# Optimization experiments

Hardware: AMD Instinct MI355X
Metric: run time of the kernel (lower is better)

The kernel has to match this reference:

```python
import jax, jax.numpy as jnp
import numpy as np

FEATURE_DIM = 512
NUM_HEADS = 8
HEAD_DIM = FEATURE_DIM // NUM_HEADS


def setup_inputs() -> dict:
    key = jax.random.key(0)
    ks = jax.random.split(key, 16)
    B, N, F = 16, 768, FEATURE_DIM
    Nb = N // 3
    s = 1.0 / np.sqrt(F)
    inp = {
        "x_1": jax.random.normal(ks[0], (B, N, F), jnp.float32),
        "x_2": jax.random.normal(ks[1], (B, N, F), jnp.float32),
        "z_b": jax.random.normal(ks[2], (Nb, F), jnp.float32),
        # weights stored [in, out] (torch Linear applies x @ W.T)
        "Wqkv_i": jax.random.normal(ks[3], (F, 3 * F), jnp.float32) * s,
        "Wqkv_j": jax.random.normal(ks[4], (F, 3 * F), jnp.float32) * s,
        "Wqkv_b": jax.random.normal(ks[5], (F, 3 * F), jnp.float32) * s,
        "W_f": jax.random.normal(ks[6], (2 * F, F), jnp.float32) * s,
        "b_f": jnp.zeros((F,), jnp.float32),
        "W_m": jax.random.normal(ks[7], (F, F), jnp.float32) * s,
        "b_m": jnp.zeros((F,), jnp.float32),
        "W_QKV": jax.random.normal(ks[8], (F, 3 * F), jnp.float32) * s,
        "W_proj": jax.random.normal(ks[9], (F, F), jnp.float32) * s,
        "b_proj": jnp.zeros((F,), jnp.float32),
    }
    return inp


def reference(x_1, x_2, z_b, Wqkv_i, Wqkv_j, Wqkv_b, W_f, b_f, W_m, b_m, W_QKV, W_proj, b_proj):
    z_i, z_j = x_1, x_2
    B, N, F = z_i.shape
    Nb = z_b.shape[0]
    scale = F ** -0.5           # full-dim attention scale
    Scale = HEAD_DIM ** -0.5    # multi-head attention scale

    zb = jnp.broadcast_to((z_b * 0.2)[None], (B, Nb, F))

    def split_qkv(x, W):
        qkv = (x @ W).reshape(x.shape[0], x.shape[1], 3, F)
        return qkv[:, :, 0], qkv[:, :, 1], qkv[:, :, 2]

    _, k_i, v_i = split_qkv(z_i, Wqkv_i)
    q_j, _, _ = split_qkv(z_j, Wqkv_j)
    q_b, k_b, v_b = split_qkv(zb, Wqkv_b)

    # bottleneck cross attentions (single-head, full feature dim)
    a_ib = jax.nn.softmax(jnp.einsum('bmf,bnf->bmn', q_b, k_i) * scale, axis=-1)  # [B,Nb,N]
    a_bj = jax.nn.softmax(jnp.einsum('bnf,bmf->bnm', q_j, k_b) * scale, axis=-1)  # [B,N,Nb]

    a_ib = jnp.einsum('bmn,bnf->bmf', a_ib, v_i)  # [B,Nb,F]
    attn_up = jax.nn.softmax(jnp.einsum('bnf,bmf->bnm', z_i, a_ib) * scale, axis=-1)  # [B,N,Nb]
    a_ib = jnp.einsum('bnm,bmf->bnf', attn_up, a_ib)  # [B,N,F]
    a_bj = jnp.einsum('bnm,bmf->bnf', a_bj, v_b)      # [B,N,F]
    a_ij = (a_ib + a_bj) * 0.5

    # gated fusion
    f_ij = jax.nn.sigmoid(jnp.concatenate([a_ij, z_j], axis=-1) @ W_f + b_f)
    h_ij = jax.nn.relu(z_i + (a_ij @ W_m + b_m) * f_ij)

    # standard multi-head self-attention
    QKV = (h_ij @ W_QKV).reshape(B, N, 3, NUM_HEADS, HEAD_DIM)
    Q, K, V = [jnp.transpose(QKV[:, :, t], (0, 2, 1, 3)) for t in range(3)]  # [B,H,N,hd]
    Attn = jax.nn.softmax(jnp.einsum('bhnd,bhmd->bhnm', Q, K) * Scale, axis=-1)
    H = jnp.einsum('bhnm,bhmd->bhnd', Attn, V)
    H = jnp.transpose(H, (0, 2, 1, 3)).reshape(B, N, F)
    return H @ W_proj + b_proj
```

## Files before the change

### kernel.cpp

```cpp
#include <hip/hip_runtime.h>
#include <hip/hip_bf16.h>

typedef __attribute__((ext_vector_type(8))) short short8;
typedef __attribute__((ext_vector_type(4))) float f32x4;
typedef __hip_bfloat16 bf16;
typedef unsigned short ushort;

__device__ __forceinline__ ushort f2b(float v) {
    bf16 h = __float2bfloat16(v);
    return *reinterpret_cast<ushort*>(&h);
}
__device__ __forceinline__ float b2f(ushort u) {
    return __uint_as_float((unsigned)u << 16);
}

#define GLD16(lds, gp) __builtin_amdgcn_global_load_lds( \
    (const __attribute__((address_space(1))) void*)(gp), \
    (__attribute__((address_space(3))) void*)(lds), 16, 0, 0)

__device__ __forceinline__ void xcd_swizzle(int& bx, int& by) {
    if ((gridDim.y & 7) == 0) {
        const int id = bx + gridDim.x * by;
        const int xcd = id & 7, slot = id >> 3;
        by = xcd * (gridDim.y >> 3) + slot / gridDim.x;
        bx = slot - (slot / gridDim.x) * gridDim.x;
    }
}

template<typename OutT, int EPI, int TM>
__global__ __launch_bounds__(256) void gemm_bf16(
    const bf16* __restrict__ A, const bf16* __restrict__ B, OutT* __restrict__ C,
    int K, int lda, int ldb, int ldc, long sA, long sB, long sC,
    float alpha, const float* __restrict__ bias,
    int lda2, long sA2, int eld, long sE,
    bf16* __restrict__ px, bf16* __restrict__ py, int nry)
{
    constexpr int RT = TM / 32;
    constexpr int PLA = TM * 32;
    constexpr int PLB = 128 * 32;
    constexpr int NP = (TM == 64) ? 4 : 2;
    __shared__ __align__(16) bf16 As[NP * PLA];
    __shared__ __align__(16) bf16 Bs[NP * PLB];

    const int t = threadIdx.x;
    const int w = t >> 6, lane = t & 63;
    const int wr = w >> 1, wc = w & 1;
    const int lr = lane & 15, kc4 = lane >> 4;
    const int qr = lane >> 2;
    const int kcr = ((lane & 3) - ((lane >> 3) & 3)) & 3;
    int bx = blockIdx.x, by = blockIdx.y;
    xcd_swizzle(bx, by);
    int zidx, row0;
    if (nry > 0) { zidx = by / nry; row0 = (by % nry) * TM; }
    else         { zidx = blockIdx.z; row0 = by * TM; }
    const int col0 = bx * 128;

    const bf16* Ab = A + (size_t)zidx * sA + (size_t)row0 * lda;
    const bf16* Bb = B + (size_t)zidx * sB + (size_t)col0 * ldb;

    const bf16* ga0; const bf16* ga1 = nullptr;
    if constexpr (TM == 64) {
        ga0 = Ab + (size_t)(w * 16 + qr) * lda + kcr * 8;
    } else {
        ga0 = Ab + (size_t)(w * 32 + qr) * lda + kcr * 8;
        ga1 = Ab + (size_t)(w * 32 + 16 + qr) * lda + kcr * 8;
    }
    const bf16* gb0 = Bb + (size_t)(w * 32 + qr) * ldb + kcr * 8;
    const bf16* gb1 = Bb + (size_t)(w * 32 + 16 + qr) * ldb + kcr * 8;
    bf16* lA0; bf16* lA1 = nullptr;
    if constexpr (TM == 64) { lA0 = &As[w * 512]; }
    else                    { lA0 = &As[w * 1024]; lA1 = &As[w * 1024 + 512]; }
    bf16* lB0 = &Bs[w * 1024];
    bf16* lB1 = &Bs[w * 1024 + 512];

    f32x4 acc[RT][4] = {};

    const int cSw = ((kc4 + ((lr >> 1) & 3)) & 3) * 8;
    const bf16* ApBase = &As[(wr * (TM / 2) + lr) * 32 + cSw];
    const bf16* BpBase = &Bs[(wc * 64 + lr) * 32 + cSw];

    auto stageP = [&](int plane, int ko) {
        GLD16(lA0 + plane * PLA, ga0 + ko);
        if constexpr (TM == 128) GLD16(lA1 + plane * PLA, ga1 + ko);
        GLD16(lB0 + plane * PLB, gb0 + ko);
        GLD16(lB1 + plane * PLB, gb1 + ko);
    };
    auto compP = [&](int plane) {
        const bf16* Ap = ApBase + plane * PLA;
        const bf16* Bp = BpBase + plane * PLB;
        short8 af[RT], bfr[4];
#pragma unroll
        for (int i = 0; i < RT; ++i) af[i]  = *(const short8*)(Ap + i * 512);
#pragma unroll
        for (int j = 0; j < 4; ++j) bfr[j] = *(const short8*)(Bp + j * 512);
#pragma unroll
        for (int i = 0; i < RT; ++i)
#pragma unroll
            for (int j = 0; j < 4; ++j)
                acc[i][j] = __builtin_amdgcn_mfma_f32_16x16x32_bf16(af[i], bfr[j], acc[i][j], 0, 0, 0);
    };

    if constexpr (TM == 64) {
        stageP(0, 0); stageP(1, 32);
        int buf = 0;
        for (int k0 = 0; k0 < K; k0 += 64) {
            __syncthreads();
            if (k0 + 64 < K) {
                stageP((buf ^ 1) * 2,     k0 + 64);
                stageP((buf ^ 1) * 2 + 1, k0 + 96);
            }
            compP(buf * 2); compP(buf * 2 + 1);
            buf ^= 1;
        }
    } else {
        stageP(0, 0);
        int buf = 0;
        for (int k0 = 0; k0 < K; k0 += 32) {
            __syncthreads();
            if (k0 + 32 < K) stageP(buf ^ 1, k0 + 32);
            compP(buf);
            buf ^= 1;
        }
    }

    if constexpr (EPI == 4) {
        const int sec = bx >> 2;
        const int h0 = (bx & 3) * 2;
        const int b  = by / 6;
        const int n0 = (by % 6) * TM;
        bf16* dq = (bf16*)C;
#pragma unroll
        for (int j = 0; j < 4; ++j) {
            const int col = wc * 64 + j * 16 + lr;
            const int h = h0 + (col >> 6), hd = col & 63;
            const size_t bh = (size_t)b * 8 + h;
#pragma unroll
            for (int i = 0; i < RT; ++i) {
                const int n = n0 + wr * (TM / 2) + i * 16 + kc4 * 4;
                if (sec == 2) {
                    __align__(8) ushort o[4];
#pragma unroll
                    for (int r = 0; r < 4; ++r) o[r] = f2b(acc[i][j][r]);
                    *(int2*)&py[(bh * 64 + hd) * 768 + n] = *(const int2*)o;
                } else {
                    bf16* d = (sec == 0) ? dq : px;
#pragma unroll
                    for (int r = 0; r < 4; ++r)
                        d[(bh * 768 + n + r) * 64 + hd] = __float2bfloat16(acc[i][j][r]);
                }
            }
        }
        return;
    } else if constexpr (EPI == 5) {
        const int b  = by / 6;
        const int n0 = (by % 6) * TM;
#pragma unroll
        for (int j = 0; j < 4; ++j) {
            const int col = col0 + wc * 64 + j * 16 + lr;
#pragma unroll
            for (int i = 0; i < RT; ++i) {
                const int n = n0 + wr * (TM / 2) + i * 16 + kc4 * 4;
                if (col < 512) {
#pragma unroll
                    for (int r = 0; r < 4; ++r)
                        ((bf16*)C)[((size_t)b * 768 + n + r) * 512 + col] = __float2bfloat16(acc[i][j][r]);
                } else {
                    __align__(8) ushort o[4];
#pragma unroll
                    for (int r = 0; r < 4; ++r) o[r] = f2b(acc[i][j][r]);
                    *(int2*)&py[((size_t)b * 512 + (col - 512)) * 768 + n] = *(const int2*)o;
                }
            }
        }
        return;
    }

    OutT* Cb = C + (size_t)zidx * sC;
#pragma unroll
    for (int j = 0; j < 4; ++j) {
        const int col = col0 + wc * 64 + j * 16 + lr;
        const float bv = bias ? bias[col] : 0.f;
#pragma unroll
        for (int i = 0; i < RT; ++i) {
            const int rb = row0 + wr * (TM / 2) + i * 16 + kc4 * 4;
            if constexpr (EPI == 6) {
                __align__(8) ushort o[4];
#pragma unroll
                for (int r = 0; r < 4; ++r) {
                    o[r] = f2b(alpha * acc[i][j][r]);
                    Cb[(size_t)(rb + r) * ldc + col] = __float2bfloat16(alpha * acc[i][j][r]);
                }
                *(int2*)&py[(size_t)zidx * sE + (size_t)col * eld + rb] = *(const int2*)o;
            } else if constexpr (EPI == 8) {
                __align__(8) ushort o[4];
#pragma unroll
                for (int r = 0; r < 4; ++r) {
                    o[r] = f2b(acc[i][j][r]);
                    Cb[(size_t)(rb + r) * ldc + col] = __float2bfloat16(acc[i][j][r]);
                }
                if (col >= 1024) {
                    const size_t tb = (size_t)(col - 1024) * 512 + 256 + rb;
#pragma unroll
                    for (int b2 = 0; b2 < 16; ++b2)
                        *(int2*)&py[(size_t)b2 * sE + tb] = *(const int2*)o;
                }
            } else {
#pragma unroll
                for (int r = 0; r < 4; ++r) {
                    const int row = rb + r;
                    float v = alpha * acc[i][j][r] + bv;
                    if constexpr (sizeof(OutT) == 2)
                        Cb[(size_t)row * ldc + col] = __float2bfloat16(v);
                    else
                        Cb[(size_t)row * ldc + col] = v;
                }
            }
        }
    }
}

__global__ __launch_bounds__(256) void gemm_sm(
    const bf16* __restrict__ A0, const bf16* __restrict__ B0,
    const bf16* __restrict__ A1, const bf16* __restrict__ B1,
    bf16* __restrict__ Y, float alpha)
{
    constexpr int PLA = 64 * 32;
    constexpr int PLB = 256 * 32;
    __shared__ __align__(16) bf16 As[2 * PLA];
    __shared__ __align__(16) bf16 Bs[2 * PLB];
    __shared__ float sc[2][2][2][32];

    const int t = threadIdx.x;
    const int w = t >> 6, lane = t & 63;
    const int wr = w >> 1, wc = w & 1;
    const int lr = lane & 15, kc4 = lane >> 4;
    const int qr = lane >> 2;
    const int kcr = ((lane & 3) - ((lane >> 3) & 3)) & 3;
    int bx = blockIdx.x, by = blockIdx.y;
    xcd_swizzle(bx, by);
    const int b = by / 12, row0 = (by % 12) * 64;
    const int half = blockIdx.z;

    const bf16* Ab; int lda; const bf16* Bb;
    if (half == 0) {
        Ab = A0 + (size_t)b * (768L * 512) + (size_t)row0 * 512;  lda = 512;
        Bb = B0 + (size_t)b * (256L * 512);
    } else {
        Ab = A1 + (size_t)b * (768L * 1024) + (size_t)row0 * 1024; lda = 1024;
        Bb = B1;
    }

    const bf16* ga0 = Ab + (size_t)(w * 16 + qr) * lda + kcr * 8;
    const bf16* gb0 = Bb + (size_t)(w * 32 + qr) * 512 + kcr * 8;
    const bf16* gb1 = Bb + (size_t)(w * 32 + 16 + qr) * 512 + kcr * 8;
    const bf16* gb2 = Bb + (size_t)(128 + w * 32 + qr) * 512 + kcr * 8;
    const bf16* gb3 = Bb + (size_t)(128 + w * 32 + 16 + qr) * 512 + kcr * 8;
    bf16* lA0 = &As[w * 512];
    bf16* lB0 = &Bs[w * 1024];        bf16* lB1 = &Bs[w * 1024 + 512];
    bf16* lB2 = &Bs[4096 + w * 1024]; bf16* lB3 = &Bs[4096 + w * 1024 + 512];

    f32x4 acc[2][8] = {};

    const int cSw = ((kc4 + ((lr >> 1) & 3)) & 3) * 8;
    const bf16* ApBase = &As[(wr * 32 + lr) * 32 + cSw];
    const bf16* BpBase = &Bs[(wc * 128 + lr) * 32 + cSw];

    auto stageP = [&](int pl, int ko) {
        GLD16(lA0 + pl * PLA, ga0 + ko);
        GLD16(lB0 + pl * PLB, gb0 + ko); GLD16(lB1 + pl * PLB, gb1 + ko);
        GLD16(lB2 + pl * PLB, gb2 + ko); GLD16(lB3 + pl * PLB, gb3 + ko);
    };
    auto compP = [&](int pl) {
        const bf16* Ap = ApBase + pl * PLA;
        const bf16* Bp = BpBase + pl * PLB;
        short8 af[2], bfr[8];
#pragma unroll
        for (int i = 0; i < 2; ++i) af[i] = *(const short8*)(Ap + i * 512);
#pragma unroll
        for (int j = 0; j < 8; ++j) bfr[j] = *(const short8*)(Bp + j * 512);
#pragma unroll
        for (int i = 0; i < 2; ++i)
#pragma unroll
            for (int j = 0; j < 8; ++j)
                acc[i][j] = __builtin_amdgcn_mfma_f32_16x16x32_bf16(af[i], bfr[j], acc[i][j], 0, 0, 0);
    };

    stageP(0, 0);
    int buf = 0;
    for (int k0 = 0; k0 < 512; k0 += 32) {
        __syncthreads();
        if (k0 + 32 < 512) stageP(buf ^ 1, k0 + 32);
        compP(buf);
        buf ^= 1;
    }

    float mloc[2][4], sloc[2][4], scl[2][4];
#pragma unroll
    for (int i = 0; i < 2; ++i)
#pragma unroll
        for (int e = 0; e < 4; ++e) {
            float m = alpha * acc[i][0][e];
#pragma unroll
            for (int j = 1; j < 8; ++j) m = fmaxf(m, alpha * acc[i][j][e]);
#pragma unroll
            for (int o = 1; o < 16; o <<= 1) m = fmaxf(m, __shfl_xor(m, o));
            mloc[i][e] = m;
            float s = 0.f;
#pragma unroll
            for (int j = 0; j < 8; ++j) {
                const float p = __expf(alpha * acc[i][j][e] - m);
                acc[i][j][e] = p;
                s += p;
            }
#pragma unroll
            for (int o = 1; o < 16; o <<= 1) s += __shfl_xor(s, o);
            sloc[i][e] = s;
            if (lr == 0) {
                sc[wr][wc][0][i * 16 + kc4 * 4 + e] = m;
                sc[wr][wc][1][i * 16 + kc4 * 4 + e] = s;
            }
        }
    __syncthreads();
#pragma unroll
    for (int i = 0; i < 2; ++i)
#pragma unroll
        for (int e = 0; e < 4; ++e) {
            const float m2 = sc[wr][wc ^ 1][0][i * 16 + kc4 * 4 + e];
            const float s2 = sc[wr][wc ^ 1][1][i * 16 + kc4 * 4 + e];
            const float M = fmaxf(mloc[i][e], m2);
            const float S = sloc[i][e] * __expf(mloc[i][e] - M) + s2 * __expf(m2 - M);
            scl[i][e] = __expf(mloc[i][e] - M) / S;
        }
    bf16* dst = Y + ((size_t)b * 768 + row0) * 512 + half * 256 + wc * 128;
#pragma unroll
    for (int i = 0; i < 2; ++i)
#pragma unroll
        for (int j = 0; j < 8; ++j)
#pragma unroll
            for (int e = 0; e < 4; ++e)
                dst[(size_t)(wr * 32 + i * 16 + kc4 * 4 + e) * 512 + j * 16 + lr] =
                    __float2bfloat16(acc[i][j][e] * scl[i][e]);
}

__global__ __launch_bounds__(256) void gemm_gate(
    const bf16* __restrict__ A, const bf16* __restrict__ Bf,
    const bf16* __restrict__ Bm, bf16* __restrict__ Cout,
    const float* __restrict__ bias_f, const float* __restrict__ bias_m,
    const bf16* __restrict__ x1b)
{
    constexpr int AHW = 64 * 32;
    constexpr int BHW = 128 * 32;
    __shared__ __align__(16) bf16 As[2 * AHW];
    __shared__ __align__(16) bf16 FsS[2 * BHW];
    __shared__ __align__(16) bf16 MsS[2 * BHW];

    const int t = threadIdx.x;
    const int w = t >> 6, lane = t & 63;
    const int lr = lane & 15, kc4 = lane >> 4;
    const int qr = lane >> 2;
    const int kcr = ((lane & 3) - ((lane >> 3) & 3)) & 3;
    int bx = blockIdx.x, by = blockIdx.y;
    xcd_swizzle(bx, by);
    const int row0 = by * 64, col0 = bx * 128;

    const bf16* ga0 = A  + (size_t)(row0 + w * 16 + qr) * 1024 + kcr * 8;
    const bf16* gf0 = Bf + (size_t)(col0 + w * 32 + qr) * 1024 + kcr * 8;
    const bf16* gf1 = Bf + (size_t)(col0 + w * 32 + 16 + qr) * 1024 + kcr * 8;
    const bf16* gm0 = Bm + (size_t)(col0 + w * 32 + qr) * 512 + kcr * 8;
    const bf16* gm1 = Bm + (size_t)(col0 + w * 32 + 16 + qr) * 512 + kcr * 8;
    bf16* lA0 = &As[w * 512];
    bf16* lF0 = &FsS[w * 1024]; bf16* lF1 = &FsS[w * 1024 + 512];
    bf16* lM0 = &MsS[w * 1024]; bf16* lM1 = &MsS[w * 1024 + 512];

    f32x4 acc1[4][2] = {};
    f32x4 acc2[4][2] = {};

    const int cSw = ((kc4 + ((lr >> 1) & 3)) & 3) * 8;
    const bf16* ApBase = &As[lr * 32 + cSw];
    const bf16* FpBase = &FsS[(w * 32 + lr) * 32 + cSw];
    const bf16* MpBase = &MsS[(w * 32 + lr) * 32 + cSw];

    GLD16(lA0, ga0);
    GLD16(lF0, gf0); GLD16(lF1, gf1);
    GLD16(lM0, gm0); GLD16(lM1, gm1);

    auto step = [&](int kk, int rd, int st) {
        __syncthreads();
        const int kn = kk + 32;
        if (kn < 1024) {
            GLD16(lA0 + st * AHW, ga0 + kn);
            GLD16(lF0 + st * BHW, gf0 + kn);
            GLD16(lF1 + st * BHW, gf1 + kn);
            if (kn < 512) {
                GLD16(lM0 + st * BHW, gm0 + kn);
                GLD16(lM1 + st * BHW, gm1 + kn);
            }
        }
        const bf16* Ap = ApBase + rd * AHW;
        const bf16* Fp = FpBase + rd * BHW;
        short8 af[4], ff[2];
#pragma unroll
        for (int i = 0; i < 4; ++i) af[i] = *(const short8*)(Ap + i * 512);
#pragma unroll
        for (int j = 0; j < 2; ++j) ff[j] = *(const short8*)(Fp + j * 512);
#pragma unroll
        for (int i = 0; i < 4; ++i)
#pragma unroll
            for (int j = 0; j < 2; ++j)
                acc1[i][j] = __builtin_amdgcn_mfma_f32_16x16x32_bf16(af[i], ff[j], acc1[i][j], 0, 0, 0);
        if (kk < 512) {
            const bf16* Mp = MpBase + rd * BHW;
            short8 mf[2];
#pragma unroll
            for (int j = 0; j < 2; ++j) mf[j] = *(const short8*)(Mp + j * 512);
#pragma unroll
            for (int i = 0; i < 4; ++i)
#pragma unroll
                for (int j = 0; j < 2; ++j)
                    acc2[i][j] = __builtin_amdgcn_mfma_f32_16x16x32_bf16(af[i], mf[j], acc2[i][j], 0, 0, 0);
        }
    };

    for (int k0 = 0; k0 < 1024; k0 += 64) {
        step(k0, 0, 1);
        step(k0 + 32, 1, 0);
    }

    const ushort* xr = (const ushort*)x1b;
#pragma unroll
    for (int j = 0; j < 2; ++j) {
        const int col = col0 + w * 32 + j * 16 + lr;
        const float bvf = bias_f[col], bvm = bias_m[col];
#pragma unroll
        for (int i = 0; i < 4; ++i) {
            const int rb = row0 + i * 16 + kc4 * 4;
#pragma unroll
            for (int r = 0; r < 4; ++r) {
                const int row = rb + r;
                const float sig = 1.f / (1.f + __expf(-(acc1[i][j][r] + bvf)));
                const float rr = b2f(xr[(size_t)row * 512 + col]) + (acc2[i][j][r] + bvm) * sig;
                Cout[(size_t)row * 512 + col] = __float2bfloat16(rr > 0.f ? rr : 0.f);
            }
        }
    }
}

template<typename TI, int NSRC>
__global__ __launch_bounds__(256) void k_transpose(
    const TI* __restrict__ s0, const TI* __restrict__ s1,
    const TI* __restrict__ s2, const TI* __restrict__ s3,
    bf16* __restrict__ dst, int src_ld, int dst_ld, long sSrc, long sDst,
    int rep, long repStride)
{
    __shared__ float tile[64][65];
    const int t = threadIdx.x;
    const int c0 = blockIdx.x * 64, r0 = blockIdx.y * 64;
    const int z = blockIdx.z;
    const TI* src = s0;
    if (NSRC > 1) src = (z == 0) ? s0 : (z == 1) ? s1 : (z == 2) ? s2 : s3;
    {
        const int r = t >> 2, cq = (t & 3) * 16;
        const TI* sp = src + (size_t)z * sSrc + (size_t)(r0 + r) * src_ld + c0 + cq;
        if constexpr (sizeof(TI) == 4) {
#pragma unroll
            for (int u = 0; u < 16; u += 4) {
                float4 v = *(const float4*)((const float*)sp + u);
                tile[r][cq + u]     = v.x; tile[r][cq + u + 1] = v.y;
                tile[r][cq + u + 2] = v.z; tile[r][cq + u + 3] = v.w;
            }
        } else {
            const ushort* up = (const ushort*)sp;
            union { short8 v; ushort u[8]; } p0, p1;
            p0.v = *(const short8*)up; p1.v = *(const short8*)(up + 8);
#pragma unroll
            for (int u = 0; u < 8; ++u) {
                tile[r][cq + u]     = b2f(p0.u[u]);
                tile[r][cq + 8 + u] = b2f(p1.u[u]);
            }
        }
    }
    __syncthreads();
    const int c = t >> 2, rq = (t & 3) * 16;
    __align__(16) ushort ob[16];
#pragma unroll
    for (int u = 0; u < 16; ++u) ob[u] = f2b(tile[rq + u][c]);
    for (int rp = 0; rp < rep; ++rp) {
        bf16* dp = dst + (size_t)rp * repStride + (size_t)z * sDst + (size_t)(c0 + c) * dst_ld + r0 + rq;
        *(int4*)dp       = *(const int4*)&ob[0];
        *(int4*)(dp + 8) = *(const int4*)&ob[8];
    }
}

__global__ __launch_bounds__(256) void k_cast3(const float* __restrict__ x1,
    const float* __restrict__ x2, const float* __restrict__ zb,
    const float* __restrict__ wj,
    bf16* __restrict__ d1, bf16* __restrict__ d2, bf16* __restrict__ d3,
    bf16* __restrict__ d4)
{
    const int z = blockIdx.z;
    const float* src; bf16* dst; int ld; float scale; int n;
    if (z == 0)      { src = x1; dst = d1; ld = 512;  scale = 1.f;  n = 6291456; }
    else if (z == 1) { src = x2; dst = d2; ld = 1024; scale = 1.f;  n = 6291456; }
    else if (z == 2) { src = zb; dst = d3; ld = 512;  scale = 0.2f; n = 131072;  }
    else             { src = wj; dst = d4; ld = 512;  scale = 1.f;  n = 262144;  }
    int i = (blockIdx.x * 256 + threadIdx.x) * 8;
    if (i >= n) return;
    int si = i;
    if (z == 3) si = (i >> 9) * 1536 + (i & 511);
    float4 a = *(const float4*)(src + si), b = *(const float4*)(src + si + 4);
    __align__(16) ushort o[8];
    o[0] = f2b(a.x * scale); o[1] = f2b(a.y * scale); o[2] = f2b(a.z * scale); o[3] = f2b(a.w * scale);
    o[4] = f2b(b.x * scale); o[5] = f2b(b.y * scale); o[6] = f2b(b.z * scale); o[7] = f2b(b.w * scale);
    int row = i >> 9, col = i & 511;
    *(int4*)(dst + (size_t)row * ld + col) = *(const int4*)o;
}

template<int COLS, int MODE>
__global__ __launch_bounds__(256) void softmax_wave(const float* __restrict__ X,
                                                    bf16* __restrict__ Y)
{
    const int wv = threadIdx.x >> 6, lane = threadIdx.x & 63;
    const long row = (long)blockIdx.x * 4 + wv;
    const float* src = X + row * COLS;
    constexpr int V = COLS / 64;
    float v[V];
#pragma unroll
    for (int i = 0; i < V; ++i) v[i] = src[lane + i * 64];
    float m = v[0];
#pragma unroll
    for (int i = 1; i < V; ++i) m = fmaxf(m, v[i]);
#pragma unroll
    for (int o = 32; o; o >>= 1) m = fmaxf(m, __shfl_xor(m, o));
    float s = 0.f;
#pragma unroll
    for (int i = 0; i < V; ++i) { v[i] = __expf(v[i] - m); s += v[i]; }
#pragma unroll
    for (int o = 32; o; o >>= 1) s += __shfl_xor(s, o);
    const float inv = 1.f / s;
    bf16* dst = Y + row * COLS;
#pragma unroll
    for (int i = 0; i < V; ++i) dst[lane + i * 64] = __float2bfloat16(v[i] * inv);
}

__global__ __launch_bounds__(256) void mhsa_flash_mfma(
    const bf16* __restrict__ Qb, const bf16* __restrict__ Kb,
    const bf16* __restrict__ VT, bf16* __restrict__ Hout)
{
    constexpr int LD = 72;
    __shared__ __align__(16) ushort Qs[64 * LD];
    __shared__ __align__(16) ushort Ks[64 * LD];
    __shared__ __align__(16) ushort Vt[64 * LD];
    __shared__ __align__(16) ushort Ps[64 * LD];

    const int t = threadIdx.x;
    const int w = t >> 6, lane = t & 63;
    const int l16 = lane & 15, q4 = lane >> 4;
    const int h = blockIdx.x, b = blockIdx.y, qt = blockIdx.z;
    const size_t bh = (size_t)b * 8 + h;
    const ushort* qbase = (const ushort*)Qb + bh * 768 * 64;
    const ushort* kbase = (const ushort*)Kb + bh * 768 * 64;
    const ushort* vbase = (const ushort*)VT + bh * 64 * 768;

    const int r = t >> 2, c0 = (t & 3) * 16;

    {
        const ushort* src = qbase + (size_t)(qt * 64 + r) * 64 + c0;
        *(int4*)&Qs[r * LD + c0]     = *(const int4*)src;
        *(int4*)&Qs[r * LD + c0 + 8] = *(const int4*)(src + 8);
    }

    int4 ka0, ka1, va0, va1;
    {
        const ushort* ks = kbase + (size_t)r * 64 + c0;
        ka0 = *(const int4*)ks; ka1 = *(const int4*)(ks + 8);
        const ushort* vs = vbase + (size_t)r * 768 + c0;
        va0 = *(const int4*)vs; va1 = *(const int4*)(vs + 8);
    }
    __syncthreads();

    short8 qf0 = *(const short8*)&Qs[(w * 16 + l16) * LD + q4 * 8];
    short8 qf1 = *(const short8*)&Qs[(w * 16 + l16) * LD + 32 + q4 * 8];

    float lsum[4] = {0.f, 0.f, 0.f, 0.f};
    f32x4 acc[4] = {};

    for (int kt = 0; kt < 12; ++kt) {
        if (kt) __syncthreads();
        *(int4*)&Ks[r * LD + c0]     = ka0;
        *(int4*)&Ks[r * LD + c0 + 8] = ka1;
        *(int4*)&Vt[r * LD + c0]     = va0;
        *(int4*)&Vt[r * LD + c0 + 8] = va1;
        __syncthreads();

        if (kt < 11) {
            const ushort* ks = kbase + (size_t)((kt + 1) * 64 + r) * 64 + c0;
            ka0 = *(const int4*)ks; ka1 = *(const int4*)(ks + 8);
            const ushort* vs = vbase + (size_t)r * 768 + (kt + 1) * 64 + c0;
            va0 = *(const int4*)vs; va1 = *(const int4*)(vs + 8);
        }

        f32x4 s[4] = {};
#pragma unroll
        for (int nt = 0; nt < 4; ++nt) {
            short8 kf0 = *(const short8*)&Ks[(nt * 16 + l16) * LD + q4 * 8];
            short8 kf1 = *(const short8*)&Ks[(nt * 16 + l16) * LD + 32 + q4 * 8];
            s[nt] = __builtin_amdgcn_mfma_f32_16x16x32_bf16(qf0, kf0, s[nt], 0, 0, 0);
            s[nt] = __builtin_amdgcn_mfma_f32_16x16x32_bf16(qf1, kf1, s[nt], 0, 0, 0);
        }

#pragma unroll
        for (int nt = 0; nt < 4; ++nt) {
#pragma unroll
            for (int e = 0; e < 4; ++e) {
                const float p = __expf(s[nt][e] * 0.125f);
                lsum[e] += p;
                Ps[(w * 16 + q4 * 4 + e) * LD + nt * 16 + l16] = f2b(p);
            }
        }

        short8 pf0 = *(const short8*)&Ps[(w * 16 + l16) * LD + q4 * 8];
        short8 pf1 = *(const short8*)&Ps[(w * 16 + l16) * LD + 32 + q4 * 8];
#pragma unroll
        for (int jt = 0; jt < 4; ++jt) {
            short8 vf0 = *(const short8*)&Vt[(jt * 16 + l16) * LD + q4 * 8];
            short8 vf1 = *(const short8*)&Vt[(jt * 16 + l16) * LD + 32 + q4 * 8];
            acc[jt] = __builtin_amdgcn_mfma_f32_16x16x32_bf16(pf0, vf0, acc[jt], 0, 0, 0);
            acc[jt] = __builtin_amdgcn_mfma_f32_16x16x32_bf16(pf1, vf1, acc[jt], 0, 0, 0);
        }
    }

    const int orow = qt * 64 + w * 16 + q4 * 4;
#pragma unroll
    for (int e = 0; e < 4; ++e) {
        float l = lsum[e];
        l += __shfl_xor(l, 1);
        l += __shfl_xor(l, 2);
        l += __shfl_xor(l, 4);
        l += __shfl_xor(l, 8);
        const float inv = 1.f / l;
        const size_t rbase = ((size_t)b * 768 + orow + e) * 512 + h * 64;
#pragma unroll
        for (int jt = 0; jt < 4; ++jt)
            Hout[rbase + jt * 16 + l16] = __float2bfloat16(acc[jt][e] * inv);
    }
}

extern "C" void kernel_launch(void* const* d_in, const int* in_sizes, int n_in,
                              void* d_out, int out_size, void* d_ws, size_t ws_size,
                              hipStream_t stream)
{
    (void)in_sizes; (void)n_in; (void)out_size; (void)ws_size;
    const float* x1     = (const float*)d_in[0];
    const float* x2     = (const float*)d_in[1];
    const float* z_b    = (const float*)d_in[2];
    const float* Wqkv_i = (const float*)d_in[3];
    const float* Wqkv_j = (const float*)d_in[4];
    const float* Wqkv_b = (const float*)d_in[5];
    const float* W_f    = (const float*)d_in[6];
    const float* b_f    = (const float*)d_in[7];
    const float* W_m    = (const float*)d_in[8];
    const float* b_m    = (const float*)d_in[9];
    const float* W_QKV  = (const float*)d_in[10];
    const float* W_proj = (const float*)d_in[11];
    const float* b_proj = (const float*)d_in[12];
    float* out = (float*)d_out;

    const float scale = 0.044194173824159216f;

    char* base = (char*)d_ws;
    size_t off = 0;
    auto alloc = [&](size_t bytes) { char* r = base + off; off += (bytes + 255) & ~(size_t)255; return r; };

    char* Rq  = alloc((size_t)3 * 25165824);
    char* R1  = Rq;
    char* R2  = Rq + 25165824;
    char* R3  = Rq + 2 * 25165824;
    char* R4  = alloc(25165824);
    bf16* Wt4     = (bf16*)alloc((size_t)3 * 1536 * 512 * 2);
    bf16* Wt_f    = (bf16*)alloc(512 * 1024 * 2);
    bf16* Wt_mp   = (bf16*)alloc((size_t)2 * 512 * 512 * 2);
    bf16* Wj_bf   = (bf16*)alloc(512 * 512 * 2);
    bf16* Gbuf    = (bf16*)alloc(256 * 512 * 2);
    bf16* c_zb    = (bf16*)alloc(256 * 512 * 2);
    bf16* qkvb    = (bf16*)alloc(256 * 1536 * 2);
    bf16* aib0    = (bf16*)alloc((size_t)16 * 256 * 512 * 2);
    bf16* Bcat    = (bf16*)alloc((size_t)16 * 512 * 512 * 2);
    float* S      = (float*)alloc((size_t)16 * 256 * 768 * 4);
    bf16* Sb1     = (bf16*)alloc((size_t)16 * 256 * 768 * 2);
    bf16* Sb_cat  = (bf16*)alloc((size_t)16 * 768 * 512 * 2);
    bf16* c_cat   = (bf16*)alloc((size_t)12288 * 1024 * 2);
    bf16* hbuf    = (bf16*)alloc((size_t)12288 * 512 * 2);

    bf16* Wt_i = Wt4, *Wt_b = Wt4 + 1536 * 512,
        *Wt_qkv = Wt4 + (size_t)2 * 1536 * 512;
    bf16* Wt_m = Wt_mp, *Wt_proj = Wt_mp + 512 * 512;

    bf16*  Kc   = (bf16*)R1;
    bf16*  Qb   = (bf16*)R1;
    bf16*  Kb   = (bf16*)(R1 + 12582912);
    bf16*  v_iT = (bf16*)R2;
    bf16*  VTb  = (bf16*)R2;
    bf16*  c_x1 = (bf16*)R3;
    bf16*  Hout = (bf16*)R4;

    auto G64 = [&](const bf16* A, const bf16* B, void* C, bool outBf,
                   int M, int N, int K, int lda, int ldb, int ldc,
                   long sA, long sB, long sC, int batch, float alpha,
                   const float* bias) {
        int nry = M / 64;
        dim3 grid(N / 128, (batch > 1) ? batch * nry : nry, 1);
        if (batch == 1) nry = 0;
        if (outBf) gemm_bf16<bf16, 0, 64><<<grid, 256, 0, stream>>>(A, B, (bf16*)C, K, lda, ldb, ldc, sA, sB, sC, alpha, bias, 0, 0, 0, 0, nullptr, nullptr, nry);
        else       gemm_bf16<float, 0, 64><<<grid, 256, 0, stream>>>(A, B, (float*)C, K, lda, ldb, ldc, sA, sB, sC, alpha, bias, 0, 0, 0, 0, nullptr, nullptr, nry);
    };

    k_cast3<<<dim3(3072, 1, 4), 256, 0, stream>>>(x1, x2, z_b, Wqkv_j,
                                                  c_x1, c_cat + 512, c_zb, Wj_bf);
    k_transpose<float, 3><<<dim3(24, 8, 3), 256, 0, stream>>>(
        Wqkv_i, Wqkv_b, W_QKV, nullptr, Wt4, 1536, 512, 0, 1536L * 512, 1, 0);
    k_transpose<float, 1><<<dim3(8, 16, 1), 256, 0, stream>>>(
        W_f, nullptr, nullptr, nullptr, Wt_f, 512, 1024, 0, 0, 1, 0);
    k_transpose<float, 2><<<dim3(8, 8, 2), 256, 0, stream>>>(
        W_m, W_proj, nullptr, nullptr, Wt_mp, 512, 512, 0, 512L * 512, 1, 0);

    gemm_bf16<bf16, 8, 64><<<dim3(12, 4, 1), 256, 0, stream>>>(
        c_zb, Wt_b, qkvb, 512, 512, 512, 1536, 0, 0, 0,
        1.f, nullptr, 0, 0, 0, 512L * 512, nullptr, Bcat, 0);
    G64(qkvb + 512, Wj_bf, Gbuf, true, 256, 512, 512, 1536, 512, 512, 0, 0, 0, 1, 1.f, nullptr);
    gemm_bf16<bf16, 5, 128><<<dim3(8, 96, 1), 256, 0, stream>>>(
        c_x1, Wt_i + 512 * 512, Kc, 512, 512, 512, 512, 0, 0, 0,
        1.f, nullptr, 0, 0, 0, 0, nullptr, v_iT, 0);
    G64(qkvb, Kc, S, false, 256, 768, 512, 1536, 512, 768, 0, 768L * 512, 256L * 768, 16, scale, nullptr);
    softmax_wave<768, 0><<<1024, 256, 0, stream>>>(S, Sb1);
    gemm_bf16<bf16, 6, 64><<<dim3(4, 64, 1), 256, 0, stream>>>(
        Sb1, v_iT, aib0, 768, 768, 768, 512, 256L * 768, 512L * 768, 256L * 512,
        1.f, nullptr, 0, 0, 512, 512L * 512, nullptr, Bcat, 4);
    gemm_sm<<<dim3(1, 192, 2), 256, 0, stream>>>(c_x1, aib0, c_cat + 512, Gbuf,
                                                 Sb_cat, scale);
    G64(Sb_cat, Bcat, c_cat, true, 768, 512, 512, 512, 512, 1024,
        768L * 512, 512L * 512, 768L * 1024, 16, 0.5f, nullptr);
    gemm_gate<<<dim3(4, 192), 256, 0, stream>>>(c_cat, Wt_f, Wt_m, hbuf, b_f, b_m, c_x1);
    gemm_bf16<bf16, 4, 128><<<dim3(12, 96, 1), 256, 0, stream>>>(
        hbuf, Wt_qkv, Qb, 512, 512, 512, 0, 0, 0, 0,
        1.f, nullptr, 0, 0, 0, 0, Kb, VTb, 0);
    mhsa_flash_mfma<<<dim3(8, 16, 12), 256, 0, stream>>>(Qb, Kb, VTb, Hout);
    G64(Hout, Wt_proj, out, false, 12288, 512, 512, 512, 512, 512, 0, 0, 0, 1, 1.f, b_proj);
}
```

Before: 383.4 us.

## Load GEMM B operand directly from global memory, merge weight transposes

Adds a BD template mode to the bf16 GEMM in which the B (weight) fragments are read straight from global/L2 into registers instead of staged through LDS. This cuts LDS footprint and global-to-LDS traffic for small, heavily reused weight matrices, and the gate kernel's W_m path gets the same treatment. The three weight-transpose launches are merged into one kernel with early-exit blocks. The cost is higher global-load latency inside the MFMA loop with no prefetch, which may stall compute.

```diff
diff --git a/kernel.cpp b/kernel.cpp
--- a/kernel.cpp
+++ b/kernel.cpp
@@ -27,7 +27,7 @@
     }
 }
 
-template<typename OutT, int EPI, int TM>
+template<typename OutT, int EPI, int TM, bool BD = false>
 __global__ __launch_bounds__(256) void gemm_bf16(
     const bf16* __restrict__ A, const bf16* __restrict__ B, OutT* __restrict__ C,
     int K, int lda, int ldb, int ldc, long sA, long sB, long sC,
@@ -39,8 +39,9 @@
     constexpr int PLA = TM * 32;
     constexpr int PLB = 128 * 32;
     constexpr int NP = (TM == 64) ? 4 : 2;
+    constexpr int NBS = BD ? 16 : NP * PLB;
     __shared__ __align__(16) bf16 As[NP * PLA];
-    __shared__ __align__(16) bf16 Bs[NP * PLB];
+    __shared__ __align__(16) bf16 Bs[NBS];
 
     const int t = threadIdx.x;
     const int w = t >> 6, lane = t & 63;
@@ -70,29 +71,39 @@
     bf16* lA0; bf16* lA1 = nullptr;
     if constexpr (TM == 64) { lA0 = &As[w * 512]; }
     else                    { lA0 = &As[w * 1024]; lA1 = &As[w * 1024 + 512]; }
-    bf16* lB0 = &Bs[w * 1024];
-    bf16* lB1 = &Bs[w * 1024 + 512];
+    bf16* lB0 = nullptr; bf16* lB1 = nullptr;
+    if constexpr (!BD) { lB0 = &Bs[w * 1024]; lB1 = &Bs[w * 1024 + 512]; }
 
     f32x4 acc[RT][4] = {};
 
     const int cSw = ((kc4 + ((lr >> 1) & 3)) & 3) * 8;
     const bf16* ApBase = &As[(wr * (TM / 2) + lr) * 32 + cSw];
-    const bf16* BpBase = &Bs[(wc * 64 + lr) * 32 + cSw];
+    const bf16* BpBase = nullptr;
+    if constexpr (!BD) BpBase = &Bs[(wc * 64 + lr) * 32 + cSw];
+    const bf16* gBf = Bb + (size_t)(wc * 64 + lr) * ldb + kc4 * 8;
 
     auto stageP = [&](int plane, int ko) {
         GLD16(lA0 + plane * PLA, ga0 + ko);
         if constexpr (TM == 128) GLD16(lA1 + plane * PLA, ga1 + ko);
-        GLD16(lB0 + plane * PLB, gb0 + ko);
-        GLD16(lB1 + plane * PLB, gb1 + ko);
+        if constexpr (!BD) {
+            GLD16(lB0 + plane * PLB, gb0 + ko);
+            GLD16(lB1 + plane * PLB, gb1 + ko);
+        }
     };
-    auto compP = [&](int plane) {
+    auto compP = [&](int plane, int kk) {
         const bf16* Ap = ApBase + plane * PLA;
-        const bf16* Bp = BpBase + plane * PLB;
         short8 af[RT], bfr[4];
 #pragma unroll
         for (int i = 0; i < RT; ++i) af[i]  = *(const short8*)(Ap + i * 512);
-#pragma unroll
-        for (int j = 0; j < 4; ++j) bfr[j] = *(const short8*)(Bp + j * 512);
+        if constexpr (BD) {
+#pragma unroll
+            for (int j = 0; j < 4; ++j)
+                bfr[j] = *(const short8*)(gBf + (size_t)j * 16 * ldb + kk);
+        } else {
+            const bf16* Bp = BpBase + plane * PLB;
+#pragma unroll
+            for (int j = 0; j < 4; ++j) bfr[j] = *(const short8*)(Bp + j * 512);
+        }
 #pragma unroll
         for (int i = 0; i < RT; ++i)
 #pragma unroll
@@ -109,7 +120,7 @@
                 stageP((buf ^ 1) * 2,     k0 + 64);
                 stageP((buf ^ 1) * 2 + 1, k0 + 96);
             }
-            compP(buf * 2); compP(buf * 2 + 1);
+            compP(buf * 2, k0); compP(buf * 2 + 1, k0 + 32);
             buf ^= 1;
         }
     } else {
@@ -118,7 +129,7 @@
         for (int k0 = 0; k0 < K; k0 += 32) {
             __syncthreads();
             if (k0 + 32 < K) stageP(buf ^ 1, k0 + 32);
-            compP(buf);
+            compP(buf, k0);
             buf ^= 1;
         }
     }
@@ -352,7 +363,6 @@
     constexpr int BHW = 128 * 32;
     __shared__ __align__(16) bf16 As[2 * AHW];
     __shared__ __align__(16) bf16 FsS[2 * BHW];
-    __shared__ __align__(16) bf16 MsS[2 * BHW];
 
     const int t = threadIdx.x;
     const int w = t >> 6, lane = t & 63;
@@ -366,11 +376,8 @@
     const bf16* ga0 = A  + (size_t)(row0 + w * 16 + qr) * 1024 + kcr * 8;
     const bf16* gf0 = Bf + (size_t)(col0 + w * 32 + qr) * 1024 + kcr * 8;
     const bf16* gf1 = Bf + (size_t)(col0 + w * 32 + 16 + qr) * 1024 + kcr * 8;
-    const bf16* gm0 = Bm + (size_t)(col0 + w * 32 + qr) * 512 + kcr * 8;
-    const bf16* gm1 = Bm + (size_t)(col0 + w * 32 + 16 + qr) * 512 + kcr * 8;
     bf16* lA0 = &As[w * 512];
     bf16* lF0 = &FsS[w * 1024]; bf16* lF1 = &FsS[w * 1024 + 512];
-    bf16* lM0 = &MsS[w * 1024]; bf16* lM1 = &MsS[w * 1024 + 512];
 
     f32x4 acc1[4][2] = {};
     f32x4 acc2[4][2] = {};
@@ -378,11 +385,10 @@
     const int cSw = ((kc4 + ((lr >> 1) & 3)) & 3) * 8;
     const bf16* ApBase = &As[lr * 32 + cSw];
     const bf16* FpBase = &FsS[(w * 32 + lr) * 32 + cSw];
-    const bf16* MpBase = &MsS[(w * 32 + lr) * 32 + cSw];
+    const bf16* gMf = Bm + (size_t)(col0 + w * 32 + lr) * 512 + kc4 * 8;
 
     GLD16(lA0, ga0);
     GLD16(lF0, gf0); GLD16(lF1, gf1);
-    GLD16(lM0, gm0); GLD16(lM1, gm1);
 
     auto step = [&](int kk, int rd, int st) {
         __syncthreads();
@@ -391,10 +397,6 @@
             GLD16(lA0 + st * AHW, ga0 + kn);
             GLD16(lF0 + st * BHW, gf0 + kn);
             GLD16(lF1 + st * BHW, gf1 + kn);
-            if (kn < 512) {
-                GLD16(lM0 + st * BHW, gm0 + kn);
-                GLD16(lM1 + st * BHW, gm1 + kn);
-            }
         }
         const bf16* Ap = ApBase + rd * AHW;
         const bf16* Fp = FpBase + rd * BHW;
@@ -409,10 +411,10 @@
             for (int j = 0; j < 2; ++j)
                 acc1[i][j] = __builtin_amdgcn_mfma_f32_16x16x32_bf16(af[i], ff[j], acc1[i][j], 0, 0, 0);
         if (kk < 512) {
-            const bf16* Mp = MpBase + rd * BHW;
             short8 mf[2];
 #pragma unroll
-            for (int j = 0; j < 2; ++j) mf[j] = *(const short8*)(Mp + j * 512);
+            for (int j = 0; j < 2; ++j)
+                mf[j] = *(const short8*)(gMf + (size_t)j * 16 * 512 + kk);
 #pragma unroll
             for (int i = 0; i < 4; ++i)
 #pragma unroll
@@ -445,38 +447,34 @@
     }
 }
 
-template<typename TI, int NSRC>
-__global__ __launch_bounds__(256) void k_transpose(
-    const TI* __restrict__ s0, const TI* __restrict__ s1,
-    const TI* __restrict__ s2, const TI* __restrict__ s3,
-    bf16* __restrict__ dst, int src_ld, int dst_ld, long sSrc, long sDst,
-    int rep, long repStride)
+__global__ __launch_bounds__(256) void k_transpose_all(
+    const float* __restrict__ Wi, const float* __restrict__ Wb,
+    const float* __restrict__ Wq, const float* __restrict__ Wf,
+    const float* __restrict__ Wm, const float* __restrict__ Wp,
+    bf16* __restrict__ dWt4, bf16* __restrict__ dWf, bf16* __restrict__ dWmp)
 {
+    const int z = blockIdx.z;
+    const float* src; bf16* dst; int sld, dld, xmax, ymax;
+    if (z < 3)      { src = (z == 0) ? Wi : (z == 1) ? Wb : Wq;
+                      dst = dWt4 + (size_t)z * 1536 * 512;
+                      sld = 1536; dld = 512; xmax = 24; ymax = 8; }
+    else if (z == 3){ src = Wf; dst = dWf; sld = 512; dld = 1024; xmax = 8; ymax = 16; }
+    else            { src = (z == 4) ? Wm : Wp;
+                      dst = dWmp + (size_t)(z - 4) * 512 * 512;
+                      sld = 512; dld = 512; xmax = 8; ymax = 8; }
+    if (blockIdx.x >= (unsigned)xmax || blockIdx.y >= (unsigned)ymax) return;
+
     __shared__ float tile[64][65];
     const int t = threadIdx.x;
     const int c0 = blockIdx.x * 64, r0 = blockIdx.y * 64;
-    const int z = blockIdx.z;
-    const TI* src = s0;
-    if (NSRC > 1) src = (z == 0) ? s0 : (z == 1) ? s1 : (z == 2) ? s2 : s3;
     {
         const int r = t >> 2, cq = (t & 3) * 16;
-        const TI* sp = src + (size_t)z * sSrc + (size_t)(r0 + r) * src_ld + c0 + cq;
-        if constexpr (sizeof(TI) == 4) {
-#pragma unroll
-            for (int u = 0; u < 16; u += 4) {
-                float4 v = *(const float4*)((const float*)sp + u);
-                tile[r][cq + u]     = v.x; tile[r][cq + u + 1] = v.y;
-                tile[r][cq + u + 2] = v.z; tile[r][cq + u + 3] = v.w;
-            }
-        } else {
-            const ushort* up = (const ushort*)sp;
-            union { short8 v; ushort u[8]; } p0, p1;
-            p0.v = *(const short8*)up; p1.v = *(const short8*)(up + 8);
-#pragma unroll
-            for (int u = 0; u < 8; ++u) {
-                tile[r][cq + u]     = b2f(p0.u[u]);
-                tile[r][cq + 8 + u] = b2f(p1.u[u]);
-            }
+        const float* sp = src + (size_t)(r0 + r) * sld + c0 + cq;
+#pragma unroll
+        for (int u = 0; u < 16; u += 4) {
+            float4 v = *(const float4*)(sp + u);
+            tile[r][cq + u]     = v.x; tile[r][cq + u + 1] = v.y;
+            tile[r][cq + u + 2] = v.z; tile[r][cq + u + 3] = v.w;
         }
     }
     __syncthreads();
@@ -484,11 +482,9 @@
     __align__(16) ushort ob[16];
 #pragma unroll
     for (int u = 0; u < 16; ++u) ob[u] = f2b(tile[rq + u][c]);
-    for (int rp = 0; rp < rep; ++rp) {
-        bf16* dp = dst + (size_t)rp * repStride + (size_t)z * sDst + (size_t)(c0 + c) * dst_ld + r0 + rq;
-        *(int4*)dp       = *(const int4*)&ob[0];
-        *(int4*)(dp + 8) = *(const int4*)&ob[8];
-    }
+    bf16* dp = dst + (size_t)(c0 + c) * dld + r0 + rq;
+    *(int4*)dp       = *(const int4*)&ob[0];
+    *(int4*)(dp + 8) = *(const int4*)&ob[8];
 }
 
 __global__ __launch_bounds__(256) void k_cast3(const float* __restrict__ x1,
@@ -706,31 +702,32 @@
     auto G64 = [&](const bf16* A, const bf16* B, void* C, bool outBf,
                    int M, int N, int K, int lda, int ldb, int ldc,
                    long sA, long sB, long sC, int batch, float alpha,
-                   const float* bias) {
+                   const float* bias, bool bd) {
         int nry = M / 64;
         dim3 grid(N / 128, (batch > 1) ? batch * nry : nry, 1);
         if (batch == 1) nry = 0;
-        if (outBf) gemm_bf16<bf16, 0, 64><<<grid, 256, 0, stream>>>(A, B, (bf16*)C, K, lda, ldb, ldc, sA, sB, sC, alpha, bias, 0, 0, 0, 0, nullptr, nullptr, nry);
-        else       gemm_bf16<float, 0, 64><<<grid, 256, 0, stream>>>(A, B, (float*)C, K, lda, ldb, ldc, sA, sB, sC, alpha, bias, 0, 0, 0, 0, nullptr, nullptr, nry);
+        if (outBf) {
+            if (bd) gemm_bf16<bf16, 0, 64, true><<<grid, 256, 0, stream>>>(A, B, (bf16*)C, K, lda, ldb, ldc, sA, sB, sC, alpha, bias, 0, 0, 0, 0, nullptr, nullptr, nry);
+            else    gemm_bf16<bf16, 0, 64, false><<<grid, 256, 0, stream>>>(A, B, (bf16*)C, K, lda, ldb, ldc, sA, sB, sC, alpha, bias, 0, 0, 0, 0, nullptr, nullptr, nry);
+        } else {
+            if (bd) gemm_bf16<float, 0, 64, true><<<grid, 256, 0, stream>>>(A, B, (float*)C, K, lda, ldb, ldc, sA, sB, sC, alpha, bias, 0, 0, 0, 0, nullptr, nullptr, nry);
+            else    gemm_bf16<float, 0, 64, false><<<grid, 256, 0, stream>>>(A, B, (float*)C, K, lda, ldb, ldc, sA, sB, sC, alpha, bias, 0, 0, 0, 0, nullptr, nullptr, nry);
+        }
     };
 
     k_cast3<<<dim3(3072, 1, 4), 256, 0, stream>>>(x1, x2, z_b, Wqkv_j,
                                                   c_x1, c_cat + 512, c_zb, Wj_bf);
-    k_transpose<float, 3><<<dim3(24, 8, 3), 256, 0, stream>>>(
-        Wqkv_i, Wqkv_b, W_QKV, nullptr, Wt4, 1536, 512, 0, 1536L * 512, 1, 0);
-    k_transpose<float, 1><<<dim3(8, 16, 1), 256, 0, stream>>>(
-        W_f, nullptr, nullptr, nullptr, Wt_f, 512, 1024, 0, 0, 1, 0);
-    k_transpose<float, 2><<<dim3(8, 8, 2), 256, 0, stream>>>(
-        W_m, W_proj, nullptr, nullptr, Wt_mp, 512, 512, 0, 512L * 512, 1, 0);
+    k_transpose_all<<<dim3(24, 16, 6), 256, 0, stream>>>(
+        Wqkv_i, Wqkv_b, W_QKV, W_f, W_m, W_proj, Wt4, Wt_f, Wt_mp);
 
     gemm_bf16<bf16, 8, 64><<<dim3(12, 4, 1), 256, 0, stream>>>(
         c_zb, Wt_b, qkvb, 512, 512, 512, 1536, 0, 0, 0,
         1.f, nullptr, 0, 0, 0, 512L * 512, nullptr, Bcat, 0);
-    G64(qkvb + 512, Wj_bf, Gbuf, true, 256, 512, 512, 1536, 512, 512, 0, 0, 0, 1, 1.f, nullptr);
+    G64(qkvb + 512, Wj_bf, Gbuf, true, 256, 512, 512, 1536, 512, 512, 0, 0, 0, 1, 1.f, nullptr, true);
     gemm_bf16<bf16, 5, 128><<<dim3(8, 96, 1), 256, 0, stream>>>(
         c_x1, Wt_i + 512 * 512, Kc, 512, 512, 512, 512, 0, 0, 0,
         1.f, nullptr, 0, 0, 0, 0, nullptr, v_iT, 0);
-    G64(qkvb, Kc, S, false, 256, 768, 512, 1536, 512, 768, 0, 768L * 512, 256L * 768, 16, scale, nullptr);
+    G64(qkvb, Kc, S, false, 256, 768, 512, 1536, 512, 768, 0, 768L * 512, 256L * 768, 16, scale, nullptr, false);
     softmax_wave<768, 0><<<1024, 256, 0, stream>>>(S, Sb1);
     gemm_bf16<bf16, 6, 64><<<dim3(4, 64, 1), 256, 0, stream>>>(
         Sb1, v_iT, aib0, 768, 768, 768, 512, 256L * 768, 512L * 768, 256L * 512,
@@ -738,11 +735,11 @@
     gemm_sm<<<dim3(1, 192, 2), 256, 0, stream>>>(c_x1, aib0, c_cat + 512, Gbuf,
                                                  Sb_cat, scale);
     G64(Sb_cat, Bcat, c_cat, true, 768, 512, 512, 512, 512, 1024,
-        768L * 512, 512L * 512, 768L * 1024, 16, 0.5f, nullptr);
+        768L * 512, 512L * 512, 768L * 1024, 16, 0.5f, nullptr, true);
     gemm_gate<<<dim3(4, 192), 256, 0, stream>>>(c_cat, Wt_f, Wt_m, hbuf, b_f, b_m, c_x1);
     gemm_bf16<bf16, 4, 128><<<dim3(12, 96, 1), 256, 0, stream>>>(
         hbuf, Wt_qkv, Qb, 512, 512, 512, 0, 0, 0, 0,
         1.f, nullptr, 0, 0, 0, 0, Kb, VTb, 0);
     mhsa_flash_mfma<<<dim3(8, 16, 12), 256, 0, stream>>>(Qb, Kb, VTb, Hout);
-    G64(Hout, Wt_proj, out, false, 12288, 512, 512, 512, 512, 512, 0, 0, 0, 1, 1.f, b_proj);
-}
+    G64(Hout, Wt_proj, out, false, 12288, 512, 512, 512, 512, 512, 0, 0, 0, 1, 1.f, b_proj, true);
+}
```

Result: slower. 418.9 us (+9.3%).
